# Optimization experiments

Hardware: AMD Instinct MI355X
Metric: run time of the kernel (lower is better)

## Reference

```python
import jax, jax.numpy as jnp
import numpy as np

DIM = 1024
NUM_HEADS = 16
HEAD_DIM = DIM // NUM_HEADS
SCALE = HEAD_DIM ** -0.5
HIDDEN = int(DIM * 1.0)


def setup_inputs() -> dict:
    key = jax.random.key(0)
    ks = jax.random.split(key, 11)
    s = 0.02
    return {
        "x":  jax.random.normal(ks[0], (2, 2048, DIM), jnp.float32),
        "Wq": jax.random.normal(ks[1], (DIM, DIM), jnp.float32) * s,
        "bq": jnp.zeros((DIM,), jnp.float32),
        "Wk": jax.random.normal(ks[2], (DIM, DIM), jnp.float32) * s,
        "bk": jnp.zeros((DIM,), jnp.float32),
        "Wv": jax.random.normal(ks[3], (DIM, DIM), jnp.float32) * s,
        "bv": jnp.zeros((DIM,), jnp.float32),
        "W1": jax.random.normal(ks[4], (HIDDEN, DIM), jnp.float32) * s,
        "b1": jnp.zeros((HIDDEN,), jnp.float32),
        "W2": jax.random.normal(ks[5], (DIM, HIDDEN), jnp.float32) * s,
        "b2": jnp.zeros((DIM,), jnp.float32),
    }


def _split_heads(t, B, S):
    # [B,S,C] -> [B,H,S,hd]
    return t.reshape(B, S, NUM_HEADS, HEAD_DIM).transpose(0, 2, 1, 3)


def reference(x, Wq, bq, Wk, bk, Wv, bv, W1, b1, W2, b2):
    B, S, C = x.shape
    q = _split_heads(x @ Wq.T + bq, B, S) * SCALE
    k = _split_heads(x @ Wk.T + bk, B, S)
    v = _split_heads(x @ Wv.T + bv, B, S)
    # softmax-free bilinear attention, scores in float32 (matches .float())
    attn = jnp.einsum('bhqd,bhkd->bhqk', q.astype(jnp.float32), k.astype(jnp.float32))
    out = jnp.einsum('bhqk,bhkd->bhqd', attn, v)  # [B,H,S,hd]
    out = out.transpose(0, 2, 1, 3).reshape(B, S, C)
    h = jax.nn.gelu(out @ W1.T + b1, approximate=False)
    mlp = h @ W2.T + b2
    return x + out + mlp
```

## Files before the change

### kernel.cpp

```cpp
#include <hip/hip_runtime.h>
#include <math.h>

#define DIM    1024
#define BATCH  2
#define SEQ    2048
#define NHEAD  16
#define HDIM   64
#define MROWS  (BATCH*SEQ)
#define NSPLIT 8

typedef unsigned short u16;
typedef __attribute__((ext_vector_type(8))) short  s16x8;
typedef __attribute__((ext_vector_type(4))) float  f32x4;

typedef __attribute__((address_space(3))) unsigned int       lds_u32_t;
typedef const __attribute__((address_space(1))) unsigned int glb_u32_t;

__device__ __forceinline__ float bf2f(u16 h) {
    unsigned u = ((unsigned)h) << 16; float f; __builtin_memcpy(&f, &u, 4); return f;
}
__device__ __forceinline__ u16 f2bf(float f) {
    unsigned u; __builtin_memcpy(&u, &f, 4);
    u += 0x7FFFu + ((u >> 16) & 1u);
    return (u16)(u >> 16);
}

__global__ __launch_bounds__(256)
void pack_all(const float* __restrict__ x,
              const float* __restrict__ Wq, const float* __restrict__ Wk,
              const float* __restrict__ Wv, const float* __restrict__ W1,
              const float* __restrict__ W2,
              u16* __restrict__ xb, u16* __restrict__ Wqb, u16* __restrict__ Wkb,
              u16* __restrict__ Wvb, u16* __restrict__ W1b, u16* __restrict__ W2b)
{
    const int bid = blockIdx.x;
    const float* src; u16* dst; int i;
    if (bid < 4096) { src = x; dst = xb; i = bid * 256 + threadIdx.x; }
    else {
        const int w = (bid - 4096) >> 10;
        const int lb = (bid - 4096) & 1023;
        src = (w == 0) ? Wq : (w == 1) ? Wk : (w == 2) ? Wv : (w == 3) ? W1 : W2;
        dst = (w == 0) ? Wqb : (w == 1) ? Wkb : (w == 2) ? Wvb : (w == 3) ? W1b : W2b;
        i = lb * 256 + threadIdx.x;
    }
    float4 v = ((const float4*)src)[i];
    ushort4 o = { f2bf(v.x), f2bf(v.y), f2bf(v.z), f2bf(v.w) };
    ((ushort4*)dst)[i] = o;
}

__device__ __forceinline__ void gemm_core8(const u16* __restrict__ Ab,
                                           const u16* __restrict__ Bb,
                                           u16* As, u16* Bs, int tid,
                                           f32x4 acc[2][4])
{
    const int w  = tid >> 6, l = tid & 63;
    const int wm = (w >> 1) * 32, wn = (w & 1) * 64;
    const int lr = l & 15, kq = l >> 4;
    const int row = tid >> 2, cg = tid & 3;

    for (int k0 = 0; k0 < DIM; k0 += 32) {
        const u16* srcA = Ab + (size_t)row * DIM + k0 + cg * 8;
        const u16* srcB = Bb + (size_t)row * DIM + k0 + cg * 8;
        __builtin_amdgcn_global_load_lds((glb_u32_t*)srcA, (lds_u32_t*)(As + tid * 8), 16, 0, 0);
        __builtin_amdgcn_global_load_lds((glb_u32_t*)srcB, (lds_u32_t*)(Bs + tid * 8), 16, 0, 0);
        __syncthreads();
        s16x8 af[2], bfr[4];
        #pragma unroll
        for (int i = 0; i < 2; ++i)
            af[i]  = *(const s16x8*)(As + (wm + i * 16 + lr) * 32 + kq * 8);
        #pragma unroll
        for (int j = 0; j < 4; ++j)
            bfr[j] = *(const s16x8*)(Bs + (wn + j * 16 + lr) * 32 + kq * 8);
        #pragma unroll
        for (int i = 0; i < 2; ++i)
            #pragma unroll
            for (int j = 0; j < 4; ++j)
                acc[i][j] = __builtin_amdgcn_mfma_f32_16x16x32_bf16(af[i], bfr[j], acc[i][j], 0, 0, 0);
        __syncthreads();
    }
}

__global__ __launch_bounds__(512)
void qkv_gemm(const u16* __restrict__ xb,
              const u16* __restrict__ Wq, const u16* __restrict__ Wk, const u16* __restrict__ Wv,
              const float* __restrict__ bq, const float* __restrict__ bk, const float* __restrict__ bv,
              u16* __restrict__ qo, u16* __restrict__ ko, u16* __restrict__ vo)
{
    __shared__ u16 As[128 * 32];
    __shared__ u16 Bs[128 * 32];
    const int tid = threadIdx.x;
    const int sel = blockIdx.x >> 3;
    const int n0  = (blockIdx.x & 7) * 128;
    const int m0  = blockIdx.y * 128;
    const u16*   B    = (sel == 0) ? Wq : (sel == 1) ? Wk : Wv;
    const float* bias = (sel == 0) ? bq : (sel == 1) ? bk : bv;
    u16*         C    = (sel == 0) ? qo : (sel == 1) ? ko : vo;
    const float scale = (sel == 0) ? 0.125f : 1.0f;

    f32x4 acc[2][4];
    #pragma unroll
    for (int i = 0; i < 2; ++i)
        #pragma unroll
        for (int j = 0; j < 4; ++j) acc[i][j] = (f32x4){0.f, 0.f, 0.f, 0.f};

    gemm_core8(xb + (size_t)m0 * DIM, B + (size_t)n0 * DIM, As, Bs, tid, acc);

    const int w = tid >> 6, l = tid & 63;
    const int wm = (w >> 1) * 32, wn = (w & 1) * 64;
    const int er = l >> 4, ec = l & 15;
    #pragma unroll
    for (int j = 0; j < 4; ++j) {
        const int n = n0 + wn + j * 16 + ec;
        const float bb = bias[n];
        #pragma unroll
        for (int i = 0; i < 2; ++i)
            #pragma unroll
            for (int r = 0; r < 4; ++r) {
                const int m = m0 + wm + i * 16 + er * 4 + r;
                C[(size_t)m * DIM + n] = f2bf((acc[i][j][r] + bb) * scale);
            }
    }
}

__global__ __launch_bounds__(512)
void gemm_bf16(const u16* __restrict__ A, const u16* __restrict__ B,
               const float* __restrict__ bias,
               u16* __restrict__ Cb, float* __restrict__ Cf,
               const float* __restrict__ rx, const u16* __restrict__ rattn,
               int mode)
{
    __shared__ u16 As[128 * 32];
    __shared__ u16 Bs[128 * 32];
    const int tid = threadIdx.x;
    const int n0 = blockIdx.x * 128, m0 = blockIdx.y * 128;

    f32x4 acc[2][4];
    #pragma unroll
    for (int i = 0; i < 2; ++i)
        #pragma unroll
        for (int j = 0; j < 4; ++j) acc[i][j] = (f32x4){0.f, 0.f, 0.f, 0.f};

    gemm_core8(A + (size_t)m0 * DIM, B + (size_t)n0 * DIM, As, Bs, tid, acc);

    const int w = tid >> 6, l = tid & 63;
    const int wm = (w >> 1) * 32, wn = (w & 1) * 64;
    const int er = l >> 4, ec = l & 15;
    #pragma unroll
    for (int j = 0; j < 4; ++j) {
        const int n = n0 + wn + j * 16 + ec;
        const float bb = bias[n];
        #pragma unroll
        for (int i = 0; i < 2; ++i)
            #pragma unroll
            for (int r = 0; r < 4; ++r) {
                const int m = m0 + wm + i * 16 + er * 4 + r;
                const size_t idx = (size_t)m * DIM + n;
                float v = acc[i][j][r] + bb;
                if (mode == 1) {
                    v = 0.5f * v * (1.0f + erff(v * 0.70710678118654752f));
                    Cb[idx] = f2bf(v);
                } else {
                    Cf[idx] = v + rx[idx] + bf2f(rattn[idx]);
                }
            }
    }
}

__global__ __launch_bounds__(256)
void ktv_mfma(const u16* __restrict__ Kb, const u16* __restrict__ Vb,
              float* __restrict__ part)
{
    __shared__ u16 Kt[64 * 264];
    __shared__ u16 Vt[64 * 264];
    const int tid = threadIdx.x;
    const int bh = blockIdx.x & 31;
    const int sp = blockIdx.x >> 5;
    const int b = bh >> 4, h = bh & 15;
    const size_t base = (size_t)b * SEQ * DIM + (size_t)h * HDIM + (size_t)sp * 256 * DIM;

    const int dg = (tid & 15) * 4;
    #pragma unroll
    for (int pass = 0; pass < 16; ++pass) {
        const int s = (tid >> 4) + 16 * pass;
        ushort4 kv = *(const ushort4*)(Kb + base + (size_t)s * DIM + dg);
        ushort4 vv = *(const ushort4*)(Vb + base + (size_t)s * DIM + dg);
        Kt[(dg + 0) * 264 + s] = kv.x; Kt[(dg + 1) * 264 + s] = kv.y;
        Kt[(dg + 2) * 264 + s] = kv.z; Kt[(dg + 3) * 264 + s] = kv.w;
        Vt[(dg + 0) * 264 + s] = vv.x; Vt[(dg + 1) * 264 + s] = vv.y;
        Vt[(dg + 2) * 264 + s] = vv.z; Vt[(dg + 3) * 264 + s] = vv.w;
    }
    __syncthreads();

    const int w = tid >> 6, l = tid & 63;
    const int lr = l & 15, kq = l >> 4;
    f32x4 acc[4];
    #pragma unroll
    for (int j = 0; j < 4; ++j) acc[j] = (f32x4){0.f, 0.f, 0.f, 0.f};

    for (int k0 = 0; k0 < 256; k0 += 32) {
        s16x8 af = *(const s16x8*)(Kt + (w * 16 + lr) * 264 + k0 + kq * 8);
        #pragma unroll
        for (int j = 0; j < 4; ++j) {
            s16x8 bf = *(const s16x8*)(Vt + (j * 16 + lr) * 264 + k0 + kq * 8);
            acc[j] = __builtin_amdgcn_mfma_f32_16x16x32_bf16(af, bf, acc[j], 0, 0, 0);
        }
    }

    float* dst = part + ((size_t)sp * 32 + bh) * (HDIM * HDIM);
    const int er = l >> 4, ec = l & 15;
    #pragma unroll
    for (int j = 0; j < 4; ++j)
        #pragma unroll
        for (int r = 0; r < 4; ++r)
            dst[(w * 16 + er * 4 + r) * HDIM + j * 16 + ec] = acc[j][r];
}

__global__ __launch_bounds__(256)
void qktv_kernel(const u16* __restrict__ Qb, const float* __restrict__ part,
                 u16* __restrict__ attnb)
{
    __shared__ float KV[HDIM * HDIM];
    __shared__ u16 Qs[128 * 68];
    const int tid = threadIdx.x;
    const int h  = blockIdx.x;
    const int mt = blockIdx.y;
    const int row0 = mt * 128;
    const int b = row0 >> 11;
    const int bh = b * NHEAD + h;

    for (int i = tid; i < HDIM * HDIM; i += 256) {
        float s = 0.f;
        #pragma unroll
        for (int sp = 0; sp < NSPLIT; ++sp)
            s += part[((size_t)sp * 32 + bh) * (HDIM * HDIM) + i];
        KV[i] = s;
    }
    const int dg = (tid & 15) * 4;
    #pragma unroll
    for (int pass = 0; pass < 8; ++pass) {
        const int r = (tid >> 4) + 16 * pass;
        ushort4 q = *(const ushort4*)(Qb + (size_t)(row0 + r) * DIM + h * HDIM + dg);
        *(ushort4*)(Qs + r * 68 + dg) = q;
    }
    __syncthreads();

    const int tr = tid >> 3, tc = tid & 7;
    const int r0 = tr * 4, c0 = tc * 8;
    float acc[4][8] = {};
    for (int d = 0; d < HDIM; ++d) {
        float4 ka = *(const float4*)&KV[d * HDIM + c0];
        float4 kb2 = *(const float4*)&KV[d * HDIM + c0 + 4];
        const float* k8a = (const float*)&ka;
        const float* k8b = (const float*)&kb2;
        float qv[4];
        #pragma unroll
        for (int i = 0; i < 4; ++i) qv[i] = bf2f(Qs[(r0 + i) * 68 + d]);
        #pragma unroll
        for (int i = 0; i < 4; ++i)
            #pragma unroll
            for (int j = 0; j < 4; ++j) {
                acc[i][j]     += qv[i] * k8a[j];
                acc[i][j + 4] += qv[i] * k8b[j];
            }
    }
    #pragma unroll
    for (int i = 0; i < 4; ++i) {
        u16* dst = attnb + (size_t)(row0 + r0 + i) * DIM + h * HDIM + c0;
        ushort4 o0 = { f2bf(acc[i][0]), f2bf(acc[i][1]), f2bf(acc[i][2]), f2bf(acc[i][3]) };
        ushort4 o1 = { f2bf(acc[i][4]), f2bf(acc[i][5]), f2bf(acc[i][6]), f2bf(acc[i][7]) };
        *(ushort4*)(dst)     = o0;
        *(ushort4*)(dst + 4) = o1;
    }
}

extern "C" void kernel_launch(void* const* d_in, const int* in_sizes, int n_in,
                              void* d_out, int out_size, void* d_ws, size_t ws_size,
                              hipStream_t stream)
{
    const float* x  = (const float*)d_in[0];
    const float* Wq = (const float*)d_in[1];
    const float* bq = (const float*)d_in[2];
    const float* Wk = (const float*)d_in[3];
    const float* bk = (const float*)d_in[4];
    const float* Wv = (const float*)d_in[5];
    const float* bv = (const float*)d_in[6];
    const float* W1 = (const float*)d_in[7];
    const float* b1 = (const float*)d_in[8];
    const float* W2 = (const float*)d_in[9];
    const float* b2 = (const float*)d_in[10];
    float* out = (float*)d_out;

    char* ws = (char*)d_ws;
    const size_t MB = 1u << 20;
    u16* xb   = (u16*)(ws);
    u16* Wqb  = (u16*)(ws +  8 * MB);
    u16* Wkb  = (u16*)(ws + 10 * MB);
    u16* Wvb  = (u16*)(ws + 12 * MB);
    u16* W1b  = (u16*)(ws + 14 * MB);
    u16* W2b  = (u16*)(ws + 16 * MB);
    u16* qb   = (u16*)(ws + 18 * MB);
    u16* kb   = (u16*)(ws + 26 * MB);
    u16* vb   = (u16*)(ws + 34 * MB);
    float* part = (float*)(ws + 42 * MB);
    u16* attnb = kb;
    u16* h1b   = vb;

    pack_all<<<4096 + 5 * 1024, 256, 0, stream>>>(x, Wq, Wk, Wv, W1, W2,
                                                  xb, Wqb, Wkb, Wvb, W1b, W2b);

    qkv_gemm<<<dim3(24, 32), 512, 0, stream>>>(xb, Wqb, Wkb, Wvb, bq, bk, bv, qb, kb, vb);

    ktv_mfma<<<NSPLIT * 32, 256, 0, stream>>>(kb, vb, part);
    qktv_kernel<<<dim3(NHEAD, MROWS / 128), 256, 0, stream>>>(qb, part, attnb);

    gemm_bf16<<<dim3(8, 32), 512, 0, stream>>>(attnb, W1b, b1, h1b, nullptr, nullptr, nullptr, 1);
    gemm_bf16<<<dim3(8, 32), 512, 0, stream>>>(h1b, W2b, b2, nullptr, out, x, attnb, 2);
}
```

Measured before the change: 209.2 us.

## Double-buffer GEMM LDS tiles with 64-wide K steps and 4x4 warp tiles

Replaces the single-buffered 32-wide-K GEMM core with a double-buffered core. It prefetches the next 64-wide K slab into a second LDS buffer while MFMAs run on the current one, so there is one barrier per iteration instead of two. Blocks shrink from 512 to 256 threads, and each wave now computes a 64x64 tile (4x4 MFMA fragments), raising register reuse per LDS load. The costs are more accumulator registers per thread, 64KB of LDS per block (lower occupancy), and fewer waves available to hide latency.

After: 253.1 us. 1.21x slower.

```diff
diff --git a/kernel.cpp b/kernel.cpp
--- a/kernel.cpp
+++ b/kernel.cpp
@@ -48,46 +48,68 @@
     ((ushort4*)dst)[i] = o;
 }
 
-__device__ __forceinline__ void gemm_core8(const u16* __restrict__ Ab,
-                                           const u16* __restrict__ Bb,
-                                           u16* As, u16* Bs, int tid,
-                                           f32x4 acc[2][4])
-{
-    const int w  = tid >> 6, l = tid & 63;
-    const int wm = (w >> 1) * 32, wn = (w & 1) * 64;
+__device__ __forceinline__ void stage64(const u16* __restrict__ g, int k0,
+                                        u16* lds, int tid)
+{
+    #pragma unroll
+    for (int j = 0; j < 4; ++j) {
+        const int cid = j * 256 + tid;
+        const int p   = cid >> 9;
+        const int r   = (cid >> 2) & 127;
+        const int c2  = cid & 3;
+        const u16* src = g + (size_t)r * DIM + k0 + p * 32 + c2 * 8;
+        __builtin_amdgcn_global_load_lds((glb_u32_t*)src,
+                                         (lds_u32_t*)(lds + (size_t)cid * 8), 16, 0, 0);
+    }
+}
+
+__device__ __forceinline__ void gemm_core_db(const u16* __restrict__ Ab,
+                                             const u16* __restrict__ Bb,
+                                             u16* As, u16* Bs,
+                                             int tid, f32x4 acc[4][4])
+{
+    const int w = tid >> 6, l = tid & 63;
+    const int wm = (w >> 1) * 64, wn = (w & 1) * 64;
     const int lr = l & 15, kq = l >> 4;
-    const int row = tid >> 2, cg = tid & 3;
-
-    for (int k0 = 0; k0 < DIM; k0 += 32) {
-        const u16* srcA = Ab + (size_t)row * DIM + k0 + cg * 8;
-        const u16* srcB = Bb + (size_t)row * DIM + k0 + cg * 8;
-        __builtin_amdgcn_global_load_lds((glb_u32_t*)srcA, (lds_u32_t*)(As + tid * 8), 16, 0, 0);
-        __builtin_amdgcn_global_load_lds((glb_u32_t*)srcB, (lds_u32_t*)(Bs + tid * 8), 16, 0, 0);
+
+    stage64(Ab, 0, As, tid);
+    stage64(Bb, 0, Bs, tid);
+
+    for (int it = 0; it < DIM / 64; ++it) {
+        const int cur = it & 1;
+        u16* Ac = As + cur * 8192;
+        u16* Bc = Bs + cur * 8192;
         __syncthreads();
-        s16x8 af[2], bfr[4];
-        #pragma unroll
-        for (int i = 0; i < 2; ++i)
-            af[i]  = *(const s16x8*)(As + (wm + i * 16 + lr) * 32 + kq * 8);
-        #pragma unroll
-        for (int j = 0; j < 4; ++j)
-            bfr[j] = *(const s16x8*)(Bs + (wn + j * 16 + lr) * 32 + kq * 8);
-        #pragma unroll
-        for (int i = 0; i < 2; ++i)
+        if (it + 1 < DIM / 64) {
+            stage64(Ab, (it + 1) * 64, As + (cur ^ 1) * 8192, tid);
+            stage64(Bb, (it + 1) * 64, Bs + (cur ^ 1) * 8192, tid);
+        }
+        #pragma unroll
+        for (int ks = 0; ks < 2; ++ks) {
+            s16x8 af[4], bfr[4];
+            #pragma unroll
+            for (int i = 0; i < 4; ++i)
+                af[i]  = *(const s16x8*)(Ac + ks * 4096 + (wm + i * 16 + lr) * 32 + kq * 8);
             #pragma unroll
             for (int j = 0; j < 4; ++j)
-                acc[i][j] = __builtin_amdgcn_mfma_f32_16x16x32_bf16(af[i], bfr[j], acc[i][j], 0, 0, 0);
-        __syncthreads();
-    }
-}
-
-__global__ __launch_bounds__(512)
+                bfr[j] = *(const s16x8*)(Bc + ks * 4096 + (wn + j * 16 + lr) * 32 + kq * 8);
+            #pragma unroll
+            for (int i = 0; i < 4; ++i)
+                #pragma unroll
+                for (int j = 0; j < 4; ++j)
+                    acc[i][j] = __builtin_amdgcn_mfma_f32_16x16x32_bf16(af[i], bfr[j], acc[i][j], 0, 0, 0);
+        }
+    }
+}
+
+__global__ __launch_bounds__(256)
 void qkv_gemm(const u16* __restrict__ xb,
               const u16* __restrict__ Wq, const u16* __restrict__ Wk, const u16* __restrict__ Wv,
               const float* __restrict__ bq, const float* __restrict__ bk, const float* __restrict__ bv,
               u16* __restrict__ qo, u16* __restrict__ ko, u16* __restrict__ vo)
 {
-    __shared__ u16 As[128 * 32];
-    __shared__ u16 Bs[128 * 32];
+    __shared__ u16 As[2 * 8192];
+    __shared__ u16 Bs[2 * 8192];
     const int tid = threadIdx.x;
     const int sel = blockIdx.x >> 3;
     const int n0  = (blockIdx.x & 7) * 128;
@@ -97,23 +119,23 @@
     u16*         C    = (sel == 0) ? qo : (sel == 1) ? ko : vo;
     const float scale = (sel == 0) ? 0.125f : 1.0f;
 
-    f32x4 acc[2][4];
-    #pragma unroll
-    for (int i = 0; i < 2; ++i)
+    f32x4 acc[4][4];
+    #pragma unroll
+    for (int i = 0; i < 4; ++i)
         #pragma unroll
         for (int j = 0; j < 4; ++j) acc[i][j] = (f32x4){0.f, 0.f, 0.f, 0.f};
 
-    gemm_core8(xb + (size_t)m0 * DIM, B + (size_t)n0 * DIM, As, Bs, tid, acc);
+    gemm_core_db(xb + (size_t)m0 * DIM, B + (size_t)n0 * DIM, As, Bs, tid, acc);
 
     const int w = tid >> 6, l = tid & 63;
-    const int wm = (w >> 1) * 32, wn = (w & 1) * 64;
+    const int wm = (w >> 1) * 64, wn = (w & 1) * 64;
     const int er = l >> 4, ec = l & 15;
     #pragma unroll
     for (int j = 0; j < 4; ++j) {
         const int n = n0 + wn + j * 16 + ec;
         const float bb = bias[n];
         #pragma unroll
-        for (int i = 0; i < 2; ++i)
+        for (int i = 0; i < 4; ++i)
             #pragma unroll
             for (int r = 0; r < 4; ++r) {
                 const int m = m0 + wm + i * 16 + er * 4 + r;
@@ -122,35 +144,35 @@
     }
 }
 
-__global__ __launch_bounds__(512)
+__global__ __launch_bounds__(256)
 void gemm_bf16(const u16* __restrict__ A, const u16* __restrict__ B,
                const float* __restrict__ bias,
                u16* __restrict__ Cb, float* __restrict__ Cf,
                const float* __restrict__ rx, const u16* __restrict__ rattn,
                int mode)
 {
-    __shared__ u16 As[128 * 32];
-    __shared__ u16 Bs[128 * 32];
+    __shared__ u16 As[2 * 8192];
+    __shared__ u16 Bs[2 * 8192];
     const int tid = threadIdx.x;
     const int n0 = blockIdx.x * 128, m0 = blockIdx.y * 128;
 
-    f32x4 acc[2][4];
-    #pragma unroll
-    for (int i = 0; i < 2; ++i)
+    f32x4 acc[4][4];
+    #pragma unroll
+    for (int i = 0; i < 4; ++i)
         #pragma unroll
         for (int j = 0; j < 4; ++j) acc[i][j] = (f32x4){0.f, 0.f, 0.f, 0.f};
 
-    gemm_core8(A + (size_t)m0 * DIM, B + (size_t)n0 * DIM, As, Bs, tid, acc);
+    gemm_core_db(A + (size_t)m0 * DIM, B + (size_t)n0 * DIM, As, Bs, tid, acc);
 
     const int w = tid >> 6, l = tid & 63;
-    const int wm = (w >> 1) * 32, wn = (w & 1) * 64;
+    const int wm = (w >> 1) * 64, wn = (w & 1) * 64;
     const int er = l >> 4, ec = l & 15;
     #pragma unroll
     for (int j = 0; j < 4; ++j) {
         const int n = n0 + wn + j * 16 + ec;
         const float bb = bias[n];
         #pragma unroll
-        for (int i = 0; i < 2; ++i)
+        for (int i = 0; i < 4; ++i)
             #pragma unroll
             for (int r = 0; r < 4; ++r) {
                 const int m = m0 + wm + i * 16 + er * 4 + r;
@@ -248,7 +270,7 @@
     const int r0 = tr * 4, c0 = tc * 8;
     float acc[4][8] = {};
     for (int d = 0; d < HDIM; ++d) {
-        float4 ka = *(const float4*)&KV[d * HDIM + c0];
+        float4 ka  = *(const float4*)&KV[d * HDIM + c0];
         float4 kb2 = *(const float4*)&KV[d * HDIM + c0 + 4];
         const float* k8a = (const float*)&ka;
         const float* k8b = (const float*)&kb2;
@@ -308,11 +330,11 @@
     pack_all<<<4096 + 5 * 1024, 256, 0, stream>>>(x, Wq, Wk, Wv, W1, W2,
                                                   xb, Wqb, Wkb, Wvb, W1b, W2b);
 
-    qkv_gemm<<<dim3(24, 32), 512, 0, stream>>>(xb, Wqb, Wkb, Wvb, bq, bk, bv, qb, kb, vb);
+    qkv_gemm<<<dim3(24, 32), 256, 0, stream>>>(xb, Wqb, Wkb, Wvb, bq, bk, bv, qb, kb, vb);
 
     ktv_mfma<<<NSPLIT * 32, 256, 0, stream>>>(kb, vb, part);
     qktv_kernel<<<dim3(NHEAD, MROWS / 128), 256, 0, stream>>>(qb, part, attnb);
 
-    gemm_bf16<<<dim3(8, 32), 512, 0, stream>>>(attnb, W1b, b1, h1b, nullptr, nullptr, nullptr, 1);
-    gemm_bf16<<<dim3(8, 32), 512, 0, stream>>>(h1b, W2b, b2, nullptr, out, x, attnb, 2);
-}
+    gemm_bf16<<<dim3(8, 32), 256, 0, stream>>>(attnb, W1b, b1, h1b, nullptr, nullptr, nullptr, 1);
+    gemm_bf16<<<dim3(8, 32), 256, 0, stream>>>(h1b, W2b, b2, nullptr, out, x, attnb, 2);
+}
```
